# Kernel tuning notes

Measured on AMD Instinct MI355X. Metric: run time of the kernel, lower is better.

The kernel has to match this reference:

```python
import jax, jax.numpy as jnp
import numpy as np

P = 5.0  # p-norm order from init_kwargs


def setup_inputs() -> dict:
    key = jax.random.key(0)
    k1, k2 = jax.random.split(key)
    B, N, M, C = 8, 4096, 4096, 3
    x = jax.random.normal(k1, (B, N, C), dtype=jnp.float32)
    y = jax.random.normal(k2, (B, M, C), dtype=jnp.float32)
    return {"x": x, "y": y}


def _pnorm(v, axis):
    # (sum |v|^p)^(1/p), matching torch.norm(p=5)
    return jnp.sum(jnp.abs(v) ** P, axis=axis) ** (1.0 / P)


def reference(x, y):
    # Squared Euclidean distance matrix [B, N, M]
    d = (-2.0 * jnp.einsum("bnc,bmc->bnm", x, y)
         + jnp.sum(x * x, -1)[:, :, None]
         + jnp.sum(y * y, -1)[:, None, :])
    idx1 = jnp.argmin(d, axis=2)  # [B, N]: nearest y for each x
    idx2 = jnp.argmin(d, axis=1)  # [B, M]: nearest x for each y
    nn_y = jnp.take_along_axis(y, idx1[..., None], axis=1)  # [B, N, 3]
    nn_x = jnp.take_along_axis(x, idx2[..., None], axis=1)  # [B, M, 3]
    pc1 = _pnorm(x - nn_y, axis=-1)  # [B, N]
    pc2 = _pnorm(y - nn_x, axis=-1)  # [B, M]
    result2 = _pnorm(pc1, axis=-1) + _pnorm(pc2, axis=-1)  # [B]
    return jnp.mean(result2)
```

## Files before the change

kernel.cpp:

```cpp
#include <hip/hip_runtime.h>
#include <math.h>


#define BQ      256
#define QPT     4
#define SPLITS  16
#define CH      256
#define GS      8
#define NG      (CH / GS)
#define BIGOFF  64.0f
#define NQTOT   65536
#define NTILE   64
#define TILEQ   1024

typedef float f32x2 __attribute__((ext_vector_type(2)));
typedef float f32x4 __attribute__((ext_vector_type(4)));

static __device__ __forceinline__ f32x2 mk2(float s) { f32x2 v; v.x = s; v.y = s; return v; }
static __device__ __forceinline__ f32x2 fma2(f32x2 a, f32x2 b, f32x2 c) {
    return __builtin_elementwise_fma(a, b, c);
}
__device__ __forceinline__ unsigned int float_ord(float f) {
    unsigned int u = __float_as_uint(f);
    return (u & 0x80000000u) ? ~u : (u | 0x80000000u);
}

#define WS_ACC    0
#define WS_CANARY 128
#define WS_GCNT   192
#define WS_TCNT   256
#define WS_PSUM   1024
#define WS_TAB    4096
#define WS_TBL    1048576

__global__ __launch_bounds__(BQ) void chamfer_mktab(
    const float* __restrict__ x, const float* __restrict__ y,
    float4* __restrict__ tbl)
{
    const int t   = blockIdx.x * BQ + threadIdx.x;
    const int dir = t >> 14;
    const int b   = (t >> 11) & 7;
    const int pr  = t & 2047;
    const float* R = (dir == 0 ? y : x) + (size_t)b * 4096 * 3;
    const float* rp = R + (size_t)(2 * pr) * 3;
    const float f0 = rp[0], f1 = rp[1], f2 = rp[2];
    const float f3 = rp[3], f4 = rp[4], f5 = rp[5];
    const float h0 = fmaf(0.5f * f0, f0, fmaf(0.5f * f1, f1, fmaf(0.5f * f2, f2, BIGOFF)));
    const float h1 = fmaf(0.5f * f3, f3, fmaf(0.5f * f4, f4, fmaf(0.5f * f5, f5, BIGOFF)));
    const size_t o = ((size_t)(dir * 8 + b) * 2048 + pr) * 2;
    tbl[o]     = make_float4(f0, f3, f1, f4);
    tbl[o + 1] = make_float4(f2, f5, h0, h1);
}

#define COMPUTE_GROUP(BUF, G)                                              \
  {                                                                        \
    _Pragma("unroll")                                                      \
    for (int k4 = 0; k4 < 4; ++k4) {                                       \
      const f32x4 a = BUF[2 * k4];                    \
      const f32x4 c = BUF[2 * k4 + 1];                 \
      const f32x2 rx = __builtin_shufflevector(a, a, 0, 1);                \
      const f32x2 ry = __builtin_shufflevector(a, a, 2, 3);                \
      const f32x2 rz = __builtin_shufflevector(c, c, 0, 1);                \
      const f32x2 h2 = __builtin_shufflevector(c, c, 2, 3);                \
      const int jbase = ((G) * 4 + k4) * 2;                                \
      _Pragma("unroll")                                                    \
      for (int qk = 0; qk < QPT; ++qk) {                                   \
        const f32x2 s = fma2(nqx[qk], rx,                                  \
                        fma2(nqy[qk], ry, fma2(nqz[qk], rz, h2)));         \
        const float mp = fminf(s.x, s.y);                                  \
        const int   jp = jbase + ((s.x <= s.y) ? 0 : 1);    \
        const bool  cc = mp < best[qk];       \
        best[qk] = cc ? mp : best[qk];                                     \
        bj[qk]   = cc ? jp : bj[qk];                                       \
      }                                                                    \
    }                                                                      \
  }

__global__ __launch_bounds__(BQ, 4) void chamfer_fused_r15(
    const float* __restrict__ x, const float* __restrict__ y,
    const f32x4* __restrict__ tbl,
    unsigned long long* __restrict__ tab,
    unsigned int* __restrict__ tcnt, unsigned int* __restrict__ gcnt,
    const unsigned int* __restrict__ canary_p,
    float* __restrict__ psum, float* __restrict__ out)
{
    __shared__ float red[4];
    __shared__ int s_flag;

    const int bid   = blockIdx.x;
    const int split = bid & (SPLITS - 1);
    const int tq    = bid >> 4;
    const int dir   = tq >> 5;
    const int b     = (tq >> 2) & 7;
    const int t4    = tq & 3;

    const unsigned int canary = *canary_p;

    const float* Q; const float* R;
    if (dir == 0) { Q = x + (size_t)b * 4096 * 3; R = y + (size_t)b * 4096 * 3; }
    else          { Q = y + (size_t)b * 4096 * 3; R = x + (size_t)b * 4096 * 3; }

    const int tid = threadIdx.x;

    const f32x4* __restrict__ tb =
        tbl + ((size_t)(dir * 8 + b) * 4096 + (size_t)split * 256);

    f32x2 nqx[QPT], nqy[QPT], nqz[QPT];
    #pragma unroll
    for (int qk = 0; qk < QPT; ++qk) {
        const int ql = t4 * TILEQ + qk * 256 + tid;
        nqx[qk] = mk2(-Q[ql * 3 + 0]);
        nqy[qk] = mk2(-Q[ql * 3 + 1]);
        nqz[qk] = mk2(-Q[ql * 3 + 2]);
    }

    float best[QPT]; int bj[QPT];
    #pragma unroll
    for (int qk = 0; qk < QPT; ++qk) { best[qk] = 3.4e38f; bj[qk] = 0; }

    f32x4 bufA[8], bufB[8];
    #pragma unroll
    for (int i = 0; i < 8; ++i) bufA[i] = tb[i];

    #pragma unroll 1
    for (int g = 0; g < NG; g += 2) {
        #pragma unroll
        for (int i = 0; i < 8; ++i) bufB[i] = tb[(g + 1) * 8 + i];
        COMPUTE_GROUP(bufA, g)
        const int gpre = (g + 2) & (NG - 1);
        #pragma unroll
        for (int i = 0; i < 8; ++i) bufA[i] = tb[gpre * 8 + i];
        COMPUTE_GROUP(bufB, g + 1)
    }

    #pragma unroll
    for (int qk = 0; qk < QPT; ++qk) {
        const size_t qidx = (size_t)tq * TILEQ + qk * 256 + tid;
        const unsigned int jabs = (unsigned int)(split * CH + bj[qk]);
        const unsigned long long key =
            ~(((unsigned long long)__float_as_uint(best[qk]) << 32) | jabs);
        atomicMax(&tab[qidx], key);
    }

    __syncthreads();
    if (tid == 0) {
        const unsigned int old = atomicAdd(&tcnt[tq], 1u);
        s_flag = (old == canary + (SPLITS - 1));
    }
    __syncthreads();
    if (!s_flag) return;

    float sthr = 0.0f;
    #pragma unroll
    for (int k = 0; k < QPT; ++k) {
        const int gq = tq * TILEQ + k * 256 + tid;
        const int q  = t4 * TILEQ + k * 256 + tid;
        const unsigned long long w =
            ~__hip_atomic_load(&tab[gq], __ATOMIC_RELAXED, __HIP_MEMORY_SCOPE_AGENT);
        const int j = (int)(unsigned int)w;
        const float dx = Q[q * 3 + 0] - R[(size_t)j * 3 + 0];
        const float dy = Q[q * 3 + 1] - R[(size_t)j * 3 + 1];
        const float dz = Q[q * 3 + 2] - R[(size_t)j * 3 + 2];
        const float ax = fabsf(dx), ay = fabsf(dy), az = fabsf(dz);
        const float ax2 = ax * ax, ay2 = ay * ay, az2 = az * az;
        sthr += ax2 * ax2 * ax + ay2 * ay2 * ay + az2 * az2 * az;
    }
    #pragma unroll
    for (int off = 32; off > 0; off >>= 1) sthr += __shfl_down(sthr, off, 64);
    const int wid = tid >> 6, lane = tid & 63;
    if (lane == 0) red[wid] = sthr;
    __syncthreads();

    if (tid == 0) {
        __hip_atomic_store(&psum[tq], red[0] + red[1] + red[2] + red[3],
                           __ATOMIC_RELAXED, __HIP_MEMORY_SCOPE_AGENT);
        asm volatile("s_waitcnt vmcnt(0)" ::: "memory");
        const unsigned int old = atomicAdd(gcnt, 1u);
        s_flag = (old == canary + (NTILE - 1));
    }
    __syncthreads();
    if (!s_flag) return;

    if (tid < 64) {
        float v = 0.0f;
        if (tid < 16) {
            const int fb = tid >> 1, fdir = tid & 1;
            float a = 0.0f;
            #pragma unroll
            for (int t = 0; t < 4; ++t)
                a += __hip_atomic_load(&psum[fdir * 32 + fb * 4 + t],
                                       __ATOMIC_RELAXED, __HIP_MEMORY_SCOPE_AGENT);
            v = exp2f(0.2f * log2f(a));
        }
        #pragma unroll
        for (int off = 8; off > 0; off >>= 1) v += __shfl_down(v, off, 64);
        if (tid == 0) out[0] = v * 0.125f;
    }
    if (tid < NTILE)
        __hip_atomic_store(&tcnt[tid], canary, __ATOMIC_RELAXED, __HIP_MEMORY_SCOPE_AGENT);
    if (tid == 0)
        __hip_atomic_store(gcnt, canary, __ATOMIC_RELAXED, __HIP_MEMORY_SCOPE_AGENT);
}

__global__ __launch_bounds__(BQ) void chamfer_nn_split_kernel(
    const float* __restrict__ x, const float* __restrict__ y,
    unsigned long long* __restrict__ packed, int N, int M)
{
    __shared__ float4 sref[1024];
    const int bid = blockIdx.x, split = bid & 3, qb = bid >> 2;
    const int tile = qb & 15, dir = (qb >> 4) & 1, b = qb >> 5;
    const float* Q; const float* R;
    if (dir == 0) { Q = x + (size_t)b * N * 3; R = y + (size_t)b * M * 3; }
    else          { Q = y + (size_t)b * M * 3; R = x + (size_t)b * N * 3; }
    const int tid = threadIdx.x, q = tile * BQ + tid, base = split * 1024;
    for (int j = tid; j < 1024; j += BQ) {
        const float rx = R[(size_t)(base + j) * 3 + 0];
        const float ry = R[(size_t)(base + j) * 3 + 1];
        const float rz = R[(size_t)(base + j) * 3 + 2];
        sref[j] = make_float4(rx, ry, rz, 0.5f * (rx * rx + ry * ry + rz * rz));
    }
    __syncthreads();
    const float qx = Q[q * 3 + 0], qy = Q[q * 3 + 1], qz = Q[q * 3 + 2];
    float best = 3.4e38f; int bestj = base;
    #pragma unroll 8
    for (int j = 0; j < 1024; ++j) {
        const float4 r = sref[j];
        float t = __fmaf_rn(-qx, r.x, r.w);
        t = __fmaf_rn(-qy, r.y, t);
        t = __fmaf_rn(-qz, r.z, t);
        const bool c = t < best;
        best = c ? t : best; bestj = c ? (base + j) : bestj;
    }
    const size_t idx = ((size_t)dir * 8 + b) * (size_t)N + q;
    atomicMin(&packed[idx], ((unsigned long long)float_ord(best) << 32) | (unsigned int)bestj);
}

__global__ __launch_bounds__(BQ) void chamfer_gather_kernel(
    const float* __restrict__ x, const float* __restrict__ y,
    const unsigned long long* __restrict__ packed,
    float* __restrict__ acc, int N, int M)
{
    __shared__ float red[4];
    const int tid = threadIdx.x;
    const size_t gq = (size_t)blockIdx.x * BQ + tid;
    const int dir = (int)(gq / ((size_t)8 * N));
    const size_t rem = gq - (size_t)dir * 8 * N;
    const int b = (int)(rem / N), q = (int)(rem - (size_t)b * N);
    const float* Q; const float* R;
    if (dir == 0) { Q = x + (size_t)b * N * 3; R = y + (size_t)b * M * 3; }
    else          { Q = y + (size_t)b * M * 3; R = x + (size_t)b * N * 3; }
    const int j = (int)(unsigned int)packed[gq];
    const float dx = Q[q * 3 + 0] - R[(size_t)j * 3 + 0];
    const float dy = Q[q * 3 + 1] - R[(size_t)j * 3 + 1];
    const float dz = Q[q * 3 + 2] - R[(size_t)j * 3 + 2];
    const float ax = fabsf(dx), ay = fabsf(dy), az = fabsf(dz);
    const float ax2 = ax * ax, ay2 = ay * ay, az2 = az * az;
    float s = ax2 * ax2 * ax + ay2 * ay2 * ay + az2 * az2 * az;
    #pragma unroll
    for (int off = 32; off > 0; off >>= 1) s += __shfl_down(s, off, 64);
    const int wid = tid >> 6, lane = tid & 63;
    if (lane == 0) red[wid] = s;
    __syncthreads();
    if (tid == 0) atomicAdd(&acc[b * 2 + dir], red[0] + red[1] + red[2] + red[3]);
}

__global__ void chamfer_finalize_kernel(const float* __restrict__ acc,
                                        float* __restrict__ out)
{
    if (threadIdx.x == 0 && blockIdx.x == 0) {
        float total = 0.0f;
        #pragma unroll
        for (int i = 0; i < 16; ++i) total += powf(acc[i], 0.2f);
        *out = total * 0.125f;
    }
}

extern "C" void kernel_launch(void* const* d_in, const int* in_sizes, int n_in,
                              void* d_out, int out_size, void* d_ws, size_t ws_size,
                              hipStream_t stream)
{
    const float* x = (const float*)d_in[0];
    const float* y = (const float*)d_in[1];
    float* out = (float*)d_out;
    const int N = in_sizes[0] / 24;
    const int M = in_sizes[1] / 24;

    const size_t needed = WS_TBL + (1u << 20);

    if (N == 4096 && M == 4096 && ws_size >= needed) {
        unsigned char* ws = (unsigned char*)d_ws;
        unsigned long long* tab = (unsigned long long*)(ws + WS_TAB);
        unsigned int* tcnt = (unsigned int*)(ws + WS_TCNT);
        unsigned int* gcnt = (unsigned int*)(ws + WS_GCNT);
        const unsigned int* canary = (const unsigned int*)(ws + WS_CANARY);
        float* psum = (float*)(ws + WS_PSUM);
        chamfer_mktab<<<32768 / BQ, BQ, 0, stream>>>(x, y, (float4*)(ws + WS_TBL));
        chamfer_fused_r15<<<NTILE * SPLITS, BQ, 0, stream>>>(
            x, y, (const f32x4*)(ws + WS_TBL), tab, tcnt, gcnt, canary, psum, out);
    } else {
        unsigned char* ws = (unsigned char*)d_ws;
        float* acc = (float*)ws;
        unsigned long long* ptab = (unsigned long long*)(ws + 4096);
        const size_t nQ = (size_t)2 * 8 * N;
        hipMemsetAsync(acc, 0, 64, stream);
        hipMemsetAsync(ptab, 0xFF, nQ * 8, stream);
        chamfer_nn_split_kernel<<<(int)(nQ / BQ) * 4, BQ, 0, stream>>>(x, y, ptab, N, M);
        chamfer_gather_kernel<<<(int)(nQ / BQ), BQ, 0, stream>>>(x, y, ptab, acc, N, M);
        chamfer_finalize_kernel<<<1, 64, 0, stream>>>(acc, out);
    }
}
```

Baseline: 99.15 us.

## Track per-group minimum then rescan winning group to recover nearest index

The inner loop now reduces each group of eight candidates with packed min operations and records only the best group index, instead of selecting an argmin for every candidate pair. After the scan, the winning group is recomputed from the raw reference points to find the exact index whose score equals the minimum. Queries are also processed one at a time in an outer loop, rotated by split, rather than four queries interleaved over register double-buffered table loads. This cuts compare and select instructions in the hot loop, but it reloads the table once per query, and the recomputed score must match the table-based score bit for bit or the index falls back to the group's first element.

```diff
diff --git a/kernel.cpp b/kernel.cpp
--- a/kernel.cpp
+++ b/kernel.cpp
@@ -19,6 +19,9 @@
 static __device__ __forceinline__ f32x2 mk2(float s) { f32x2 v; v.x = s; v.y = s; return v; }
 static __device__ __forceinline__ f32x2 fma2(f32x2 a, f32x2 b, f32x2 c) {
     return __builtin_elementwise_fma(a, b, c);
+}
+static __device__ __forceinline__ f32x2 min2(f32x2 a, f32x2 b) {
+    return __builtin_elementwise_min(a, b);
 }
 __device__ __forceinline__ unsigned int float_ord(float f) {
     unsigned int u = __float_as_uint(f);
@@ -52,31 +55,7 @@
     tbl[o + 1] = make_float4(f2, f5, h0, h1);
 }
 
-#define COMPUTE_GROUP(BUF, G)                                              \
-  {                                                                        \
-    _Pragma("unroll")                                                      \
-    for (int k4 = 0; k4 < 4; ++k4) {                                       \
-      const f32x4 a = BUF[2 * k4];                    \
-      const f32x4 c = BUF[2 * k4 + 1];                 \
-      const f32x2 rx = __builtin_shufflevector(a, a, 0, 1);                \
-      const f32x2 ry = __builtin_shufflevector(a, a, 2, 3);                \
-      const f32x2 rz = __builtin_shufflevector(c, c, 0, 1);                \
-      const f32x2 h2 = __builtin_shufflevector(c, c, 2, 3);                \
-      const int jbase = ((G) * 4 + k4) * 2;                                \
-      _Pragma("unroll")                                                    \
-      for (int qk = 0; qk < QPT; ++qk) {                                   \
-        const f32x2 s = fma2(nqx[qk], rx,                                  \
-                        fma2(nqy[qk], ry, fma2(nqz[qk], rz, h2)));         \
-        const float mp = fminf(s.x, s.y);                                  \
-        const int   jp = jbase + ((s.x <= s.y) ? 0 : 1);    \
-        const bool  cc = mp < best[qk];       \
-        best[qk] = cc ? mp : best[qk];                                     \
-        bj[qk]   = cc ? jp : bj[qk];                                       \
-      }                                                                    \
-    }                                                                      \
-  }
-
-__global__ __launch_bounds__(BQ, 4) void chamfer_fused_r15(
+__global__ __launch_bounds__(BQ, 4) void chamfer_fused_r16(
     const float* __restrict__ x, const float* __restrict__ y,
     const f32x4* __restrict__ tbl,
     unsigned long long* __restrict__ tab,
@@ -114,31 +93,47 @@
         nqz[qk] = mk2(-Q[ql * 3 + 2]);
     }
 
-    float best[QPT]; int bj[QPT];
-    #pragma unroll
-    for (int qk = 0; qk < QPT; ++qk) { best[qk] = 3.4e38f; bj[qk] = 0; }
-
-    f32x4 bufA[8], bufB[8];
-    #pragma unroll
-    for (int i = 0; i < 8; ++i) bufA[i] = tb[i];
-
     #pragma unroll 1
-    for (int g = 0; g < NG; g += 2) {
+    for (int qs = 0; qs < QPT; ++qs) {
+        const int qk = (qs + split) & (QPT - 1);
+        const f32x2 qnx = nqx[qk], qny = nqy[qk], qnz = nqz[qk];
+
+        float best = 3.4e38f; int bg = 0;
+        #pragma unroll 4
+        for (int g = 0; g < NG; ++g) {
+            f32x2 macc = mk2(3.4e38f);
+            #pragma unroll
+            for (int k4 = 0; k4 < 4; ++k4) {
+                const f32x4 a = tb[(g * 4 + k4) * 2];
+                const f32x4 c = tb[(g * 4 + k4) * 2 + 1];
+                const f32x2 rx = __builtin_shufflevector(a, a, 0, 1);
+                const f32x2 ry = __builtin_shufflevector(a, a, 2, 3);
+                const f32x2 rz = __builtin_shufflevector(c, c, 0, 1);
+                const f32x2 h2 = __builtin_shufflevector(c, c, 2, 3);
+                const f32x2 s = fma2(qnx, rx, fma2(qny, ry, fma2(qnz, rz, h2)));
+                macc = min2(macc, s);
+            }
+            const float m = fminf(macc.x, macc.y);
+            const bool cc = m < best;
+            best = cc ? m : best;
+            bg   = cc ? g : bg;
+        }
+
+        const float qx = -qnx.x, qy = -qny.x, qz = -qnz.x;
+        const int basej = split * CH + bg * GS;
+        int bj = basej;
         #pragma unroll
-        for (int i = 0; i < 8; ++i) bufB[i] = tb[(g + 1) * 8 + i];
-        COMPUTE_GROUP(bufA, g)
-        const int gpre = (g + 2) & (NG - 1);
-        #pragma unroll
-        for (int i = 0; i < 8; ++i) bufA[i] = tb[gpre * 8 + i];
-        COMPUTE_GROUP(bufB, g + 1)
-    }
-
-    #pragma unroll
-    for (int qk = 0; qk < QPT; ++qk) {
+        for (int j = GS - 1; j >= 0; --j) {
+            const float* rp = R + (size_t)(basej + j) * 3;
+            const float rx = rp[0], ry = rp[1], rz = rp[2];
+            const float h = fmaf(0.5f * rx, rx, fmaf(0.5f * ry, ry, fmaf(0.5f * rz, rz, BIGOFF)));
+            const float s = fmaf(-qx, rx, fmaf(-qy, ry, fmaf(-qz, rz, h)));
+            if (s == best) bj = basej + j;
+        }
+
         const size_t qidx = (size_t)tq * TILEQ + qk * 256 + tid;
-        const unsigned int jabs = (unsigned int)(split * CH + bj[qk]);
         const unsigned long long key =
-            ~(((unsigned long long)__float_as_uint(best[qk]) << 32) | jabs);
+            ~(((unsigned long long)__float_as_uint(best) << 32) | (unsigned int)bj);
         atomicMax(&tab[qidx], key);
     }
 
@@ -295,7 +290,7 @@
         const unsigned int* canary = (const unsigned int*)(ws + WS_CANARY);
         float* psum = (float*)(ws + WS_PSUM);
         chamfer_mktab<<<32768 / BQ, BQ, 0, stream>>>(x, y, (float4*)(ws + WS_TBL));
-        chamfer_fused_r15<<<NTILE * SPLITS, BQ, 0, stream>>>(
+        chamfer_fused_r16<<<NTILE * SPLITS, BQ, 0, stream>>>(
             x, y, (const f32x4*)(ws + WS_TBL), tab, tcnt, gcnt, canary, psum, out);
     } else {
         unsigned char* ws = (unsigned char*)d_ws;
```

After: 96.59 us. -2.6%, faster.
